# Kernel optimization log

Hardware: AMD Instinct MI355X
Metric: run time of the kernel (lower is better)

Reference implementation:

```python
import jax, jax.numpy as jnp
import numpy as np
from jax import lax

B, L, C = 8, 2048, 512
CR = C // 4      # SE reduction hidden
DH = C // 2      # fusion d_hidden
KS = [3, 7, 15, 20]
EPS = 1e-5


def _ln(x, g, b):
    m = jnp.mean(x, -1, keepdims=True)
    v = jnp.mean((x - m) ** 2, -1, keepdims=True)
    return (x - m) / jnp.sqrt(v + EPS) * g + b


def _bn(x, g, b, m, v):  # x: [B,C,L], eval-mode BatchNorm1d
    return (x - m[:, None]) / jnp.sqrt(v[:, None] + EPS) * g[:, None] + b[:, None]


def _forward(x, pw_w, pw_b, pw_bn_g, pw_bn_b, pw_bn_m, pw_bn_v,
             dw_w0, dw_w1, dw_w2, dw_w3, dw_b, dw_bn_g, dw_bn_b, dw_bn_m, dw_bn_v,
             se_w1, se_b1, se_w2, se_b2, se_ln_g, se_ln_b,
             df_ln_g, df_ln_b, wq, bq, wv, bv, wg, bg,
             op_w, op_b, op_ln_g, op_ln_b, fn_g, fn_b):
    Bs, Ls, Cs = x.shape
    x_in = jnp.transpose(x, (0, 2, 1))                      # [B,C,L]
    # pointwise conv (1x1) + BN + ReLU
    x_pw = jnp.einsum('oc,bcl->bol', pw_w, x_in) + pw_b[:, None]
    x_pw = jax.nn.relu(_bn(x_pw, pw_bn_g, pw_bn_b, pw_bn_m, pw_bn_v))

    enhanced = []
    for i, (w, k) in enumerate(zip([dw_w0, dw_w1, dw_w2, dw_w3], KS)):
        p = (k - 1) // 2
        y = lax.conv_general_dilated(
            x_pw, w[:, None, :], window_strides=(1,), padding=[(p, p)],
            feature_group_count=Cs, dimension_numbers=('NCH', 'OIH', 'NCH'))
        y = y + dw_b[i][:, None]
        y = jax.nn.relu(_bn(y, dw_bn_g[i], dw_bn_b[i], dw_bn_m[i], dw_bn_v[i]))
        if y.shape[2] > Ls:
            y = y[:, :, :Ls]
        elif y.shape[2] < Ls:
            y = jnp.pad(y, ((0, 0), (0, 0), (0, Ls - y.shape[2])))
        feat = jnp.transpose(y, (0, 2, 1))                  # [B,L,C]
        # ChannelAttentionBlock (SE): pool over L -> MLP -> sigmoid gate -> residual LN
        ym = jnp.mean(feat, axis=1)                          # [B,C]
        h = jax.nn.relu(ym @ se_w1[i].T + se_b1[i])          # [B,CR]
        wt = jax.nn.sigmoid(h @ se_w2[i].T + se_b2[i])       # [B,C]
        enhanced.append(_ln(feat + feat * wt[:, None, :], se_ln_g[i], se_ln_b[i]))

    # diff_conv: fixed weight w[:,:,0]=-1, w[:,:,1]=1 => every out channel is
    # sum_c(x[l+1,c]-x[l,c]); pad one zero step at the end
    s = jnp.sum(x[:, 1:] - x[:, :-1], axis=-1, keepdims=True)    # [B,L-1,1]
    diff_feat = jnp.pad(jnp.broadcast_to(s, (Bs, Ls - 1, Cs)), ((0, 0), (0, 1), (0, 0)))

    # DiffGuidedInteractiveFusion
    D = _ln(diff_feat, df_ln_g, df_ln_b)
    Q = D @ wq.T + bq                                       # [B,L,DH]
    scores = []
    for f in enhanced:
        Vi = f @ wv.T + bv                                  # [B,L,DH]
        scores.append(jnp.tanh(Q * Vi) @ wg + bg)           # [B,L]
    scores = jnp.stack(scores, axis=-1)                     # [B,L,S]
    sw = jax.nn.softmax(scores, axis=-1)
    fused = sum(sw[..., i:i + 1] * enhanced[i] for i in range(len(enhanced)))
    out = _ln(fused @ op_w.T + op_b, op_ln_g, op_ln_b)
    return _ln(out + x, fn_g, fn_b)


def setup_inputs() -> dict:
    key = jax.random.key(0)
    ks = jax.random.split(key, 12)
    r = lambda k, s: jax.random.normal(k, s, jnp.float32) * 0.02
    return {
        'x': jax.random.normal(ks[0], (B, L, C), jnp.float32),
        'pw_w': r(ks[1], (C, C)), 'pw_b': jnp.zeros(C),
        'pw_bn_g': jnp.ones(C), 'pw_bn_b': jnp.zeros(C), 'pw_bn_m': jnp.zeros(C), 'pw_bn_v': jnp.ones(C),
        'dw_w0': r(ks[2], (C, 3)), 'dw_w1': r(ks[3], (C, 7)), 'dw_w2': r(ks[4], (C, 15)), 'dw_w3': r(ks[5], (C, 20)),
        'dw_b': jnp.zeros((4, C)),
        'dw_bn_g': jnp.ones((4, C)), 'dw_bn_b': jnp.zeros((4, C)), 'dw_bn_m': jnp.zeros((4, C)), 'dw_bn_v': jnp.ones((4, C)),
        'se_w1': r(ks[6], (4, CR, C)), 'se_b1': jnp.zeros((4, CR)),
        'se_w2': r(ks[7], (4, C, CR)), 'se_b2': jnp.zeros((4, C)),
        'se_ln_g': jnp.ones((4, C)), 'se_ln_b': jnp.zeros((4, C)),
        'df_ln_g': jnp.ones(C), 'df_ln_b': jnp.zeros(C),
        'wq': r(ks[8], (DH, C)), 'bq': jnp.zeros(DH),
        'wv': r(ks[9], (DH, C)), 'bv': jnp.zeros(DH),
        'wg': r(ks[10], (DH,)), 'bg': jnp.zeros(()),
        'op_w': r(ks[11], (C, C)), 'op_b': jnp.zeros(C),
        'op_ln_g': jnp.ones(C), 'op_ln_b': jnp.zeros(C),
        'fn_g': jnp.ones(C), 'fn_b': jnp.zeros(C),
    }


def reference(x, pw_w, pw_b, pw_bn_g, pw_bn_b, pw_bn_m, pw_bn_v,
              dw_w0, dw_w1, dw_w2, dw_w3, dw_b, dw_bn_g, dw_bn_b, dw_bn_m, dw_bn_v,
              se_w1, se_b1, se_w2, se_b2, se_ln_g, se_ln_b,
              df_ln_g, df_ln_b, wq, bq, wv, bv, wg, bg,
              op_w, op_b, op_ln_g, op_ln_b, fn_g, fn_b):
    return _forward(x, pw_w, pw_b, pw_bn_g, pw_bn_b, pw_bn_m, pw_bn_v,
                    dw_w0, dw_w1, dw_w2, dw_w3, dw_b, dw_bn_g, dw_bn_b, dw_bn_m, dw_bn_v,
                    se_w1, se_b1, se_w2, se_b2, se_ln_g, se_ln_b,
                    df_ln_g, df_ln_b, wq, bq, wv, bv, wg, bg,
                    op_w, op_b, op_ln_g, op_ln_b, fn_g, fn_b)
```

## Files before the change

### kernel.cpp

```cpp
#include <hip/hip_runtime.h>
#include <math.h>

static constexpr int Bz = 8;
static constexpr int Lz = 2048;
static constexpr int Cz = 512;
static constexpr int CRz = 128;
static constexpr int DHz = 256;
static constexpr int MT = Bz * Lz;
static constexpr float EPSz = 1e-5f;

typedef unsigned short u16;
typedef __bf16 bf16x8 __attribute__((ext_vector_type(8)));
typedef float f32x4 __attribute__((ext_vector_type(4)));
typedef unsigned short u16x8 __attribute__((ext_vector_type(8)));

__device__ __forceinline__ float bf2f(u16 u) {
  unsigned int v = ((unsigned int)u) << 16;
  return __builtin_bit_cast(float, v);
}
__device__ __forceinline__ u16 f2bf(float f) {
  unsigned int b = __builtin_bit_cast(unsigned int, f);
  b += 0x7FFFu + ((b >> 16) & 1u);
  return (u16)(b >> 16);
}
__device__ __forceinline__ f32x4 mfma16(bf16x8 a, bf16x8 b, f32x4 c) {
  return __builtin_amdgcn_mfma_f32_16x16x32_bf16(a, b, c, 0, 0, 0);
}

__global__ __launch_bounds__(256) void cvt_bf16_kernel(
    const float* __restrict__ src, u16* __restrict__ dst, int n8) {
  int i = blockIdx.x * 256 + threadIdx.x;
  if (i >= n8) return;
  const float4* s = (const float4*)src;
  float4 a = s[i * 2], b = s[i * 2 + 1];
  u16x8 o;
  o[0] = f2bf(a.x); o[1] = f2bf(a.y); o[2] = f2bf(a.z); o[3] = f2bf(a.w);
  o[4] = f2bf(b.x); o[5] = f2bf(b.y); o[6] = f2bf(b.z); o[7] = f2bf(b.w);
  ((u16x8*)dst)[i] = o;
}

__global__ __launch_bounds__(256) void prep_kernel(
    const float* __restrict__ pw_b, const float* __restrict__ pw_g,
    const float* __restrict__ pw_bb, const float* __restrict__ pw_m,
    const float* __restrict__ pw_v,
    const float* __restrict__ dw_b, const float* __restrict__ dw_g,
    const float* __restrict__ dw_bb, const float* __restrict__ dw_m,
    const float* __restrict__ dw_v,
    const float* __restrict__ df_ln_b, const float* __restrict__ wq,
    const float* __restrict__ bq,
    float* __restrict__ pwA, float* __restrict__ pwB,
    float* __restrict__ dwA, float* __restrict__ dwB,
    float* __restrict__ qc) {
  const int blk = blockIdx.x;
  const int t = threadIdx.x;
  if (blk == 0) {
    for (int c = t; c < Cz; c += 256) {
      float inv = rsqrtf(pw_v[c] + EPSz);
      float a = pw_g[c] * inv;
      float bb = pw_bb[c] - pw_m[c] * a;
      pwA[c] = a;
      pwB[c] = pw_b[c] * a + bb;
    }
  } else if (blk <= 4) {
    const int i = blk - 1;
    for (int c = t; c < Cz; c += 256) {
      int idx = i * Cz + c;
      float inv = rsqrtf(dw_v[idx] + EPSz);
      float a = dw_g[idx] * inv;
      float bb = dw_bb[idx] - dw_m[idx] * a;
      dwA[idx] = a;
      dwB[idx] = dw_b[idx] * a + bb;
    }
  } else {
    if (t < DHz) {
      float s = bq[t];
      const float* w = wq + (size_t)t * Cz;
      for (int c = 0; c < Cz; c++) s += df_ln_b[c] * w[c];
      qc[t] = s;
    }
  }
}

__global__ __launch_bounds__(256, 2) void pw_mfma_kernel(
    const u16* __restrict__ Wbf, const float* __restrict__ x,
    const float* __restrict__ alpha, const float* __restrict__ beta,
    u16* __restrict__ xpw) {
  __shared__ __align__(16) char lds[74240];
  u16(*sX)[520] = (u16(*)[520])lds;
  u16(*sW)[40] = (u16(*)[40])(lds + 33280);
  u16* sC = (u16*)(lds + 33280);
  __shared__ float sAl[Cz];
  __shared__ float sBe[Cz];
  const int bat = blockIdx.x >> 6;
  const int l0 = (blockIdx.x & 63) * 32;
  const int t = threadIdx.x;
  const int lane = t & 63, w = t >> 6;
  const int fr = lane & 15, fk = (lane >> 4) * 8;
  const int mh = (w >> 1) * 16;
  const int nh = (w & 1) * 16;
#pragma unroll
  for (int rep = 0; rep < 8; rep++) {
    const int idx = rep * 256 + t;
    const int row = idx >> 6;
    const int col = (idx & 63) * 8;
    const float* src = x + ((size_t)bat * Lz + l0 + row) * Cz + col;
    float4 f0 = *(const float4*)src;
    float4 f1 = *(const float4*)(src + 4);
    u16x8 o;
    o[0] = f2bf(f0.x); o[1] = f2bf(f0.y); o[2] = f2bf(f0.z); o[3] = f2bf(f0.w);
    o[4] = f2bf(f1.x); o[5] = f2bf(f1.y); o[6] = f2bf(f1.z); o[7] = f2bf(f1.w);
    *(u16x8*)&sX[row][col] = o;
  }
  for (int c = t; c < Cz; c += 256) { sAl[c] = alpha[c]; sBe[c] = beta[c]; }
  f32x4 acc[16];
#pragma unroll
  for (int mf = 0; mf < 16; mf++)
#pragma unroll
    for (int r = 0; r < 4; r++) acc[mf][r] = 0.f;
  const int wrow = t >> 2, wch = (t & 3) * 8;
  const u16* wbase = Wbf + (size_t)wrow * Cz + wch;
  u16x8 breg[8];
#pragma unroll
  for (int rep = 0; rep < 8; rep++)
    breg[rep] = *(const u16x8*)(wbase + (size_t)rep * 64 * Cz);
  for (int k0 = 0; k0 < Cz; k0 += 32) {
    __syncthreads();
#pragma unroll
    for (int rep = 0; rep < 8; rep++)
      *(u16x8*)&sW[rep * 64 + wrow][wch] = breg[rep];
    __syncthreads();
    if (k0 + 32 < Cz) {
#pragma unroll
      for (int rep = 0; rep < 8; rep++)
        breg[rep] = *(const u16x8*)(wbase + (size_t)rep * 64 * Cz + k0 + 32);
    }
    bf16x8 bfrag = *(const bf16x8*)&sX[nh + fr][k0 + fk];
#pragma unroll
    for (int mf = 0; mf < 16; mf++) {
      bf16x8 a = *(const bf16x8*)&sW[(mh + mf) * 16 + fr][fk];
      acc[mf] = mfma16(a, bfrag, acc[mf]);
    }
  }
  __syncthreads();
#pragma unroll
  for (int mf = 0; mf < 16; mf++) {
#pragma unroll
    for (int r = 0; r < 4; r++) {
      const int o = (mh + mf) * 16 + ((lane >> 4) << 2) + r;
      const int l = nh + fr;
      float v = fmaxf(acc[mf][r] * sAl[o] + sBe[o], 0.f);
      sC[o * 40 + l] = f2bf(v);
    }
  }
  __syncthreads();
#pragma unroll
  for (int rep = 0; rep < 8; rep++) {
    const int o = rep * 64 + (t >> 2);
    const int l8 = (t & 3) * 8;
    u16x8 v = *(const u16x8*)&sC[o * 40 + l8];
    *(u16x8*)(xpw + ((size_t)(bat * Cz + o)) * Lz + l0 + l8) = v;
  }
}

template <int K>
__device__ __forceinline__ void dw_body(const float* __restrict__ row,
                                        const float* __restrict__ w,
                                        float a, float bb, int valid, int t,
                                        u16* __restrict__ dst, float& psum) {
  constexpr int P = (K - 1) / 2;
  constexpr int W = 8 + K - 1;
  float wreg[K];
#pragma unroll
  for (int j = 0; j < K; j++) wreg[j] = w[j];
  const int base = t * 8 - P;
  float win[W];
  if (base >= 0 && base + W <= Lz) {
#pragma unroll
    for (int j = 0; j < W; j++) win[j] = row[base + j];
  } else {
#pragma unroll
    for (int j = 0; j < W; j++) {
      int xi = base + j;
      win[j] = (xi >= 0 && xi < Lz) ? row[xi] : 0.f;
    }
  }
  float acc[8] = {};
#pragma unroll
  for (int jj = 0; jj < K; jj++)
#pragma unroll
    for (int o = 0; o < 8; o++) acc[o] = fmaf(wreg[jj], win[jj + o], acc[o]);
  u16x8 ov;
#pragma unroll
  for (int o = 0; o < 8; o++) {
    float v = fmaxf(acc[o] * a + bb, 0.f);
    if (t * 8 + o >= valid) v = 0.f;
    ov[o] = f2bf(v);
    psum += v;
  }
  *(u16x8*)(dst + t * 8) = ov;
}

__global__ __launch_bounds__(256) void dw_conv_kernel(
    const u16* __restrict__ xpw,
    const float* __restrict__ w0, const float* __restrict__ w1,
    const float* __restrict__ w2, const float* __restrict__ w3,
    const float* __restrict__ dwA, const float* __restrict__ dwB,
    u16* __restrict__ y, float* __restrict__ ysum) {
  __shared__ float row[Lz];
  __shared__ float wsum[4];
  const int bx = blockIdx.x;
  const int i = bx >> 12;
  const int rem = bx & 4095;
  const int b = rem >> 9;
  const int c = rem & 511;
  const int t = threadIdx.x;
  const u16* src = xpw + ((size_t)(b * Cz + c)) * Lz;
  {
    u16x8 v = ((const u16x8*)src)[t];
#pragma unroll
    for (int j = 0; j < 8; j++) row[t * 8 + j] = bf2f(v[j]);
  }
  __syncthreads();
  const float a = dwA[i * Cz + c], bb = dwB[i * Cz + c];
  u16* dst = y + ((size_t)((i * Bz + b) * Cz + c)) * Lz;
  float psum = 0.f;
  if (i == 0) {
    dw_body<3>(row, w0 + c * 3, a, bb, Lz, t, dst, psum);
  } else if (i == 1) {
    dw_body<7>(row, w1 + c * 7, a, bb, Lz, t, dst, psum);
  } else if (i == 2) {
    dw_body<15>(row, w2 + c * 15, a, bb, Lz, t, dst, psum);
  } else {
    dw_body<20>(row, w3 + c * 20, a, bb, Lz - 1, t, dst, psum);
  }
  for (int off = 32; off > 0; off >>= 1) psum += __shfl_down(psum, off, 64);
  if ((t & 63) == 0) wsum[t >> 6] = psum;
  __syncthreads();
  if (t == 0) ysum[(i * Bz + b) * Cz + c] = wsum[0] + wsum[1] + wsum[2] + wsum[3];
}

__global__ __launch_bounds__(128) void se_kernel(
    const float* __restrict__ ysum,
    const float* __restrict__ se_w1, const float* __restrict__ se_b1,
    const float* __restrict__ se_w2, const float* __restrict__ se_b2,
    float* __restrict__ sc) {
  const int i = blockIdx.x >> 3;
  const int b = blockIdx.x & 7;
  __shared__ float ym[Cz];
  __shared__ float h[CRz];
  const int t = threadIdx.x;
  const float* ys = ysum + (i * Bz + b) * Cz;
  for (int cc = t; cc < Cz; cc += 128) ym[cc] = ys[cc] * (1.f / Lz);
  __syncthreads();
  {
    const float* w1 = se_w1 + (size_t)i * CRz * Cz + (size_t)t * Cz;
    float s = se_b1[i * CRz + t];
    for (int cc = 0; cc < Cz; cc++) s += ym[cc] * w1[cc];
    h[t] = fmaxf(s, 0.f);
  }
  __syncthreads();
  for (int cc = t; cc < Cz; cc += 128) {
    const float* w2 = se_w2 + ((size_t)i * Cz + cc) * CRz;
    float s = se_b2[i * Cz + cc];
    for (int r = 0; r < CRz; r++) s += h[r] * w2[r];
    float wt = 1.f / (1.f + expf(-s));
    sc[(i * Bz + b) * Cz + cc] = 1.f + wt;
  }
}

__global__ __launch_bounds__(256) void ln_transpose_kernel(
    const u16* __restrict__ ybuf, const float* __restrict__ scv,
    const float* __restrict__ se_ln_g, const float* __restrict__ se_ln_b,
    u16* __restrict__ ebuf) {
  __shared__ float tile[32][Cz + 1];
  const size_t NBL = (size_t)Bz * Cz * Lz;
  const int i = blockIdx.y >> 3;
  const int b = blockIdx.y & 7;
  const int l0 = blockIdx.x * 32;
  const int t = threadIdx.x;
  const u16* yb = ybuf + (size_t)i * NBL + (size_t)b * Cz * Lz;
  const float* scb = scv + (i * Bz + b) * Cz;
  const float* g = se_ln_g + i * Cz;
  const float* bb = se_ln_b + i * Cz;
#pragma unroll
  for (int rep = 0; rep < 8; rep++) {
    const int idx = rep * 256 + t;
    const int c = idx >> 2;
    const int l8 = (idx & 3) * 8;
    u16x8 v = *(const u16x8*)(yb + (size_t)c * Lz + l0 + l8);
    const float scale = scb[c];
#pragma unroll
    for (int j = 0; j < 8; j++) tile[l8 + j][c] = bf2f(v[j]) * scale;
  }
  __syncthreads();
  const int wave = t >> 6, lane = t & 63;
  u16* eb = ebuf + (size_t)i * NBL + ((size_t)b * Lz + l0) * Cz;
  for (int r = wave; r < 32; r += 4) {
    float vals[8];
    float s1 = 0.f, s2 = 0.f;
#pragma unroll
    for (int j = 0; j < 8; j++) {
      float v = tile[r][lane + j * 64];
      vals[j] = v; s1 += v; s2 += v * v;
    }
    for (int off = 32; off > 0; off >>= 1) {
      s1 += __shfl_xor(s1, off, 64);
      s2 += __shfl_xor(s2, off, 64);
    }
    const float m = s1 * (1.f / Cz);
    const float var = s2 * (1.f / Cz) - m * m;
    const float inv = rsqrtf(var + EPSz);
#pragma unroll
    for (int j = 0; j < 8; j++) {
      const int cc = lane + j * 64;
      eb[(size_t)r * Cz + cc] = f2bf((vals[j] - m) * inv * g[cc] + bb[cc]);
    }
  }
}

__global__ __launch_bounds__(256) void score_mfma_kernel(
    const u16* __restrict__ e0, const u16* __restrict__ e1,
    const u16* __restrict__ e2, const u16* __restrict__ e3,
    const u16* __restrict__ wvbf, const float* __restrict__ bv,
    const float* __restrict__ qc, const float* __restrict__ wg,
    const float* __restrict__ bg, float* __restrict__ scores) {
  __shared__ u16 sA[64][40];
  __shared__ u16 sB[256][40];
  __shared__ float sP[4][64];
  const int i = blockIdx.y;
  const u16* E = (i == 0) ? e0 : (i == 1) ? e1 : (i == 2) ? e2 : e3;
  const int r0 = blockIdx.x * 64;
  const int t = threadIdx.x;
  const int lane = t & 63, w = t >> 6;
  const int srow = t >> 2, skoff = (t & 3) * 8;
  const int fr = lane & 15, fk = (lane >> 4) * 8;
  const u16* ap = E + (size_t)(r0 + srow) * Cz + skoff;
  const u16* bp = wvbf + (size_t)srow * Cz + skoff;
  f32x4 acc[4][4];
#pragma unroll
  for (int m = 0; m < 4; m++)
#pragma unroll
    for (int j = 0; j < 4; j++)
#pragma unroll
      for (int r = 0; r < 4; r++) acc[m][j][r] = 0.f;
  for (int k0 = 0; k0 < Cz; k0 += 32) {
    u16x8 av = *(const u16x8*)(ap + k0);
    u16x8 bq0 = *(const u16x8*)(bp + k0);
    u16x8 bq1 = *(const u16x8*)(bp + (size_t)64 * Cz + k0);
    u16x8 bq2 = *(const u16x8*)(bp + (size_t)128 * Cz + k0);
    u16x8 bq3 = *(const u16x8*)(bp + (size_t)192 * Cz + k0);
    __syncthreads();
    *(u16x8*)&sA[srow][skoff] = av;
    *(u16x8*)&sB[srow][skoff] = bq0;
    *(u16x8*)&sB[srow + 64][skoff] = bq1;
    *(u16x8*)&sB[srow + 128][skoff] = bq2;
    *(u16x8*)&sB[srow + 192][skoff] = bq3;
    __syncthreads();
    bf16x8 am[4], bj[4];
#pragma unroll
    for (int m = 0; m < 4; m++) am[m] = *(const bf16x8*)&sA[m * 16 + fr][fk];
#pragma unroll
    for (int j = 0; j < 4; j++)
      bj[j] = *(const bf16x8*)&sB[(w * 4 + j) * 16 + fr][fk];
#pragma unroll
    for (int m = 0; m < 4; m++)
#pragma unroll
      for (int j = 0; j < 4; j++)
        acc[m][j] = mfma16(am[m], bj[j], acc[m][j]);
  }
  float part[4][4];
#pragma unroll
  for (int m = 0; m < 4; m++)
#pragma unroll
    for (int r = 0; r < 4; r++) part[m][r] = 0.f;
#pragma unroll
  for (int j = 0; j < 4; j++) {
    const int dh = (w * 4 + j) * 16 + fr;
    const float bvn = bv[dh], qcn = qc[dh], wgn = wg[dh];
#pragma unroll
    for (int m = 0; m < 4; m++)
#pragma unroll
      for (int r = 0; r < 4; r++)
        part[m][r] += tanhf(qcn * (acc[m][j][r] + bvn)) * wgn;
  }
#pragma unroll
  for (int off = 1; off < 16; off <<= 1) {
#pragma unroll
    for (int m = 0; m < 4; m++)
#pragma unroll
      for (int r = 0; r < 4; r++)
        part[m][r] += __shfl_xor(part[m][r], off, 64);
  }
  if (fr == 0) {
#pragma unroll
    for (int m = 0; m < 4; m++)
#pragma unroll
      for (int r = 0; r < 4; r++)
        sP[w][m * 16 + ((lane >> 4) << 2) + r] = part[m][r];
  }
  __syncthreads();
  if (t < 64) {
    float s = sP[0][t] + sP[1][t] + sP[2][t] + sP[3][t] + bg[0];
    scores[(size_t)i * MT + r0 + t] = s;
  }
}

__global__ __launch_bounds__(256, 2) void op_mfma_kernel(
    const u16* __restrict__ e0, const u16* __restrict__ e1,
    const u16* __restrict__ e2, const u16* __restrict__ e3,
    const float* __restrict__ scores, const u16* __restrict__ opwbf,
    const float* __restrict__ opb, u16* __restrict__ oproj) {
  __shared__ u16 sA[32][520];
  __shared__ u16 sB[512][40];
  __shared__ float sw4[4][32];
  const int m0 = blockIdx.x * 32;
  const int t = threadIdx.x;
  const int lane = t & 63, w = t >> 6;
  const int fr = lane & 15, fk = (lane >> 4) * 8;
  const int mh = (w >> 1) * 16;
  const int nh = (w & 1) * 16;
  if (t < 32) {
    const int r = m0 + t;
    float s0 = scores[r], s1 = scores[MT + r], s2 = scores[2 * MT + r],
          s3 = scores[3 * MT + r];
    float mx = fmaxf(fmaxf(s0, s1), fmaxf(s2, s3));
    float x0 = expf(s0 - mx), x1 = expf(s1 - mx), x2 = expf(s2 - mx),
          x3 = expf(s3 - mx);
    float inv = 1.f / (x0 + x1 + x2 + x3);
    sw4[0][t] = x0 * inv; sw4[1][t] = x1 * inv;
    sw4[2][t] = x2 * inv; sw4[3][t] = x3 * inv;
  }
  __syncthreads();
#pragma unroll
  for (int rep = 0; rep < 8; rep++) {
    const int idx = rep * 256 + t;
    const int row = idx >> 6;
    const int col = (idx & 63) * 8;
    const size_t off = (size_t)(m0 + row) * Cz + col;
    u16x8 v0 = *(const u16x8*)(e0 + off);
    u16x8 v1 = *(const u16x8*)(e1 + off);
    u16x8 v2 = *(const u16x8*)(e2 + off);
    u16x8 v3 = *(const u16x8*)(e3 + off);
    const float x0 = sw4[0][row], x1 = sw4[1][row], x2 = sw4[2][row],
                x3 = sw4[3][row];
    u16x8 o;
#pragma unroll
    for (int j = 0; j < 8; j++)
      o[j] = f2bf(x0 * bf2f(v0[j]) + x1 * bf2f(v1[j]) + x2 * bf2f(v2[j]) +
                  x3 * bf2f(v3[j]));
    *(u16x8*)&sA[row][col] = o;
  }
  f32x4 acc[16];
#pragma unroll
  for (int nf = 0; nf < 16; nf++)
#pragma unroll
    for (int r = 0; r < 4; r++) acc[nf][r] = 0.f;
  const int wrow = t >> 2, wch = (t & 3) * 8;
  const u16* wbase = opwbf + (size_t)wrow * Cz + wch;
  u16x8 breg[8];
#pragma unroll
  for (int rep = 0; rep < 8; rep++)
    breg[rep] = *(const u16x8*)(wbase + (size_t)rep * 64 * Cz);
  for (int k0 = 0; k0 < Cz; k0 += 32) {
    __syncthreads();
#pragma unroll
    for (int rep = 0; rep < 8; rep++)
      *(u16x8*)&sB[rep * 64 + wrow][wch] = breg[rep];
    __syncthreads();
    if (k0 + 32 < Cz) {
#pragma unroll
      for (int rep = 0; rep < 8; rep++)
        breg[rep] = *(const u16x8*)(wbase + (size_t)rep * 64 * Cz + k0 + 32);
    }
    bf16x8 a = *(const bf16x8*)&sA[mh + fr][k0 + fk];
#pragma unroll
    for (int nf = 0; nf < 16; nf++) {
      bf16x8 b = *(const bf16x8*)&sB[(nh + nf) * 16 + fr][fk];
      acc[nf] = mfma16(a, b, acc[nf]);
    }
  }
  __syncthreads();
  u16* sC = (u16*)&sA[0][0];
#pragma unroll
  for (int nf = 0; nf < 16; nf++) {
    const int n = (nh + nf) * 16 + fr;
    const float ob = opb[n];
#pragma unroll
    for (int r = 0; r < 4; r++) {
      const int row = mh + ((lane >> 4) << 2) + r;
      sC[row * 520 + n] = f2bf(acc[nf][r] + ob);
    }
  }
  __syncthreads();
#pragma unroll
  for (int rep = 0; rep < 8; rep++) {
    const int idx = rep * 256 + t;
    const int row = idx >> 6;
    const int col = (idx & 63) * 8;
    u16x8 v = *(const u16x8*)&sC[row * 520 + col];
    *(u16x8*)(oproj + (size_t)(m0 + row) * Cz + col) = v;
  }
}

__global__ __launch_bounds__(256) void final_ln_kernel(
    const u16* __restrict__ oproj, const float* __restrict__ g1,
    const float* __restrict__ b1, const float* __restrict__ x,
    const float* __restrict__ g2, const float* __restrict__ b2,
    float* __restrict__ out) {
  const int t = threadIdx.x;
  const int row = blockIdx.x * 4 + (t >> 6);
  const int lane = t & 63;
  u16x8 av = ((const u16x8*)(oproj + (size_t)row * Cz))[lane];
  float v[8];
  float s1 = 0.f, s2 = 0.f;
#pragma unroll
  for (int j = 0; j < 8; j++) {
    v[j] = bf2f(av[j]);
    s1 += v[j]; s2 += v[j] * v[j];
  }
  for (int off = 1; off < 64; off <<= 1) {
    s1 += __shfl_xor(s1, off, 64);
    s2 += __shfl_xor(s2, off, 64);
  }
  const float m1 = s1 * (1.f / Cz);
  const float iv1 = rsqrtf(s2 * (1.f / Cz) - m1 * m1 + EPSz);
  float4 g1a = ((const float4*)g1)[lane * 2], g1b = ((const float4*)g1)[lane * 2 + 1];
  float4 b1a = ((const float4*)b1)[lane * 2], b1b = ((const float4*)b1)[lane * 2 + 1];
  const float* xr = x + (size_t)row * Cz;
  float4 xa = ((const float4*)xr)[lane * 2], xb = ((const float4*)xr)[lane * 2 + 1];
  float gv[8] = {g1a.x, g1a.y, g1a.z, g1a.w, g1b.x, g1b.y, g1b.z, g1b.w};
  float bvv[8] = {b1a.x, b1a.y, b1a.z, b1a.w, b1b.x, b1b.y, b1b.z, b1b.w};
  float xv[8] = {xa.x, xa.y, xa.z, xa.w, xb.x, xb.y, xb.z, xb.w};
  float tv[8];
  s1 = 0.f; s2 = 0.f;
#pragma unroll
  for (int j = 0; j < 8; j++) {
    tv[j] = (v[j] - m1) * iv1 * gv[j] + bvv[j] + xv[j];
    s1 += tv[j]; s2 += tv[j] * tv[j];
  }
  for (int off = 1; off < 64; off <<= 1) {
    s1 += __shfl_xor(s1, off, 64);
    s2 += __shfl_xor(s2, off, 64);
  }
  const float m2 = s1 * (1.f / Cz);
  const float iv2 = rsqrtf(s2 * (1.f / Cz) - m2 * m2 + EPSz);
  float4 g2a = ((const float4*)g2)[lane * 2], g2b = ((const float4*)g2)[lane * 2 + 1];
  float4 b2a = ((const float4*)b2)[lane * 2], b2b = ((const float4*)b2)[lane * 2 + 1];
  float g2v[8] = {g2a.x, g2a.y, g2a.z, g2a.w, g2b.x, g2b.y, g2b.z, g2b.w};
  float b2v[8] = {b2a.x, b2a.y, b2a.z, b2a.w, b2b.x, b2b.y, b2b.z, b2b.w};
  float4 oa, ob;
  oa.x = (tv[0] - m2) * iv2 * g2v[0] + b2v[0];
  oa.y = (tv[1] - m2) * iv2 * g2v[1] + b2v[1];
  oa.z = (tv[2] - m2) * iv2 * g2v[2] + b2v[2];
  oa.w = (tv[3] - m2) * iv2 * g2v[3] + b2v[3];
  ob.x = (tv[4] - m2) * iv2 * g2v[4] + b2v[4];
  ob.y = (tv[5] - m2) * iv2 * g2v[5] + b2v[5];
  ob.z = (tv[6] - m2) * iv2 * g2v[6] + b2v[6];
  ob.w = (tv[7] - m2) * iv2 * g2v[7] + b2v[7];
  float* orow = out + (size_t)row * Cz;
  ((float4*)orow)[lane * 2] = oa;
  ((float4*)orow)[lane * 2 + 1] = ob;
}

extern "C" void kernel_launch(void* const* d_in, const int* in_sizes, int n_in,
                              void* d_out, int out_size, void* d_ws,
                              size_t ws_size, hipStream_t stream) {
  const float* x = (const float*)d_in[0];
  const float* pw_w = (const float*)d_in[1];
  const float* pw_b = (const float*)d_in[2];
  const float* pw_bn_g = (const float*)d_in[3];
  const float* pw_bn_b = (const float*)d_in[4];
  const float* pw_bn_m = (const float*)d_in[5];
  const float* pw_bn_v = (const float*)d_in[6];
  const float* dw_w0 = (const float*)d_in[7];
  const float* dw_w1 = (const float*)d_in[8];
  const float* dw_w2 = (const float*)d_in[9];
  const float* dw_w3 = (const float*)d_in[10];
  const float* dw_b = (const float*)d_in[11];
  const float* dw_bn_g = (const float*)d_in[12];
  const float* dw_bn_b = (const float*)d_in[13];
  const float* dw_bn_m = (const float*)d_in[14];
  const float* dw_bn_v = (const float*)d_in[15];
  const float* se_w1 = (const float*)d_in[16];
  const float* se_b1 = (const float*)d_in[17];
  const float* se_w2 = (const float*)d_in[18];
  const float* se_b2 = (const float*)d_in[19];
  const float* se_ln_g = (const float*)d_in[20];
  const float* se_ln_b = (const float*)d_in[21];
  const float* df_ln_b = (const float*)d_in[23];
  const float* wq = (const float*)d_in[24];
  const float* bq = (const float*)d_in[25];
  const float* wv = (const float*)d_in[26];
  const float* bv = (const float*)d_in[27];
  const float* wg = (const float*)d_in[28];
  const float* bg = (const float*)d_in[29];
  const float* op_w = (const float*)d_in[30];
  const float* op_b = (const float*)d_in[31];
  const float* op_ln_g = (const float*)d_in[32];
  const float* op_ln_b = (const float*)d_in[33];
  const float* fn_g = (const float*)d_in[34];
  const float* fn_b = (const float*)d_in[35];
  float* out = (float*)d_out;

  const size_t NBL = (size_t)Bz * Cz * Lz;
  char* p = (char*)d_ws;
  u16* oproj = (u16*)p; p += NBL * 2;
  u16* xpw = (u16*)p; p += NBL * 2;
  u16* ybuf = (u16*)p; p += 4 * NBL * 2;
  u16* ebuf = (u16*)p; p += 4 * NBL * 2;
  u16* pwwbf = (u16*)p; p += (size_t)Cz * Cz * 2;
  u16* wvbf = (u16*)p; p += (size_t)DHz * Cz * 2;
  u16* opwbf = (u16*)p; p += (size_t)Cz * Cz * 2;
  float* fbuf = (float*)p;
  float* ysum = fbuf;
  float* scv = fbuf + 16384;
  float* scores = fbuf + 32768;
  float* pwA = fbuf + 98304;
  float* pwB = pwA + 512;
  float* dwA = pwB + 512;
  float* dwB = dwA + 2048;
  float* qc = dwB + 2048;

  cvt_bf16_kernel<<<Cz * Cz / 8 / 256, 256, 0, stream>>>(pw_w, pwwbf,
                                                         Cz * Cz / 8);
  cvt_bf16_kernel<<<DHz * Cz / 8 / 256, 256, 0, stream>>>(wv, wvbf,
                                                          DHz * Cz / 8);
  cvt_bf16_kernel<<<Cz * Cz / 8 / 256, 256, 0, stream>>>(op_w, opwbf,
                                                         Cz * Cz / 8);

  prep_kernel<<<6, 256, 0, stream>>>(pw_b, pw_bn_g, pw_bn_b, pw_bn_m, pw_bn_v,
                                     dw_b, dw_bn_g, dw_bn_b, dw_bn_m, dw_bn_v,
                                     df_ln_b, wq, bq, pwA, pwB, dwA, dwB, qc);

  pw_mfma_kernel<<<Bz * (Lz / 32), 256, 0, stream>>>(pwwbf, x, pwA, pwB, xpw);

  dw_conv_kernel<<<4 * Bz * Cz, 256, 0, stream>>>(xpw, dw_w0, dw_w1, dw_w2,
                                                  dw_w3, dwA, dwB, ybuf, ysum);

  se_kernel<<<32, 128, 0, stream>>>(ysum, se_w1, se_b1, se_w2, se_b2, scv);

  ln_transpose_kernel<<<dim3(Lz / 32, 4 * Bz), 256, 0, stream>>>(
      ybuf, scv, se_ln_g, se_ln_b, ebuf);

  score_mfma_kernel<<<dim3(MT / 64, 4), 256, 0, stream>>>(
      ebuf, ebuf + NBL, ebuf + 2 * NBL, ebuf + 3 * NBL, wvbf, bv, qc, wg, bg,
      scores);

  op_mfma_kernel<<<MT / 32, 256, 0, stream>>>(
      ebuf, ebuf + NBL, ebuf + 2 * NBL, ebuf + 3 * NBL, scores, opwbf, op_b,
      oproj);

  final_ln_kernel<<<MT / 4, 256, 0, stream>>>(oproj, op_ln_g, op_ln_b, x, fn_g,
                                              fn_b, out);
}
```

Before: 252.0 us.

## Compute all four depthwise conv branches per block from one shared row load

The depthwise conv kernel now runs one block per (batch, channel) and computes all four kernel-size branches from a single bf16 row staged in shared memory. Previously each branch launched its own block and reloaded the same row. The weights for all branches are staged in shared memory, and the row is padded by one word every 32 floats to cut LDS bank conflicts on the strided window reads. This removes three quarters of the xpw reads and block launches, but each block does more serial work and holds more registers, and the grid shrinks fourfold, which lowers parallelism.

Result: faster. 236.4 us (-6.2%).

```diff
diff --git a/kernel.cpp b/kernel.cpp
--- a/kernel.cpp
+++ b/kernel.cpp
@@ -163,25 +163,28 @@
 }
 
 template <int K>
-__device__ __forceinline__ void dw_body(const float* __restrict__ row,
-                                        const float* __restrict__ w,
-                                        float a, float bb, int valid, int t,
-                                        u16* __restrict__ dst, float& psum) {
+__device__ __forceinline__ float dw_branch(const float* __restrict__ row,
+                                           const float* __restrict__ wts,
+                                           float a, float bb, int valid, int t,
+                                           u16* __restrict__ dst) {
   constexpr int P = (K - 1) / 2;
   constexpr int W = 8 + K - 1;
   float wreg[K];
 #pragma unroll
-  for (int j = 0; j < K; j++) wreg[j] = w[j];
+  for (int j = 0; j < K; j++) wreg[j] = wts[j];
   const int base = t * 8 - P;
   float win[W];
   if (base >= 0 && base + W <= Lz) {
 #pragma unroll
-    for (int j = 0; j < W; j++) win[j] = row[base + j];
+    for (int j = 0; j < W; j++) {
+      const int idx = base + j;
+      win[j] = row[idx + (idx >> 5)];
+    }
   } else {
 #pragma unroll
     for (int j = 0; j < W; j++) {
-      int xi = base + j;
-      win[j] = (xi >= 0 && xi < Lz) ? row[xi] : 0.f;
+      const int idx = base + j;
+      win[j] = (idx >= 0 && idx < Lz) ? row[idx + (idx >> 5)] : 0.f;
     }
   }
   float acc[8] = {};
@@ -190,6 +193,7 @@
 #pragma unroll
     for (int o = 0; o < 8; o++) acc[o] = fmaf(wreg[jj], win[jj + o], acc[o]);
   u16x8 ov;
+  float psum = 0.f;
 #pragma unroll
   for (int o = 0; o < 8; o++) {
     float v = fmaxf(acc[o] * a + bb, 0.f);
@@ -198,6 +202,7 @@
     psum += v;
   }
   *(u16x8*)(dst + t * 8) = ov;
+  return psum;
 }
 
 __global__ __launch_bounds__(256) void dw_conv_kernel(
@@ -206,37 +211,52 @@
     const float* __restrict__ w2, const float* __restrict__ w3,
     const float* __restrict__ dwA, const float* __restrict__ dwB,
     u16* __restrict__ y, float* __restrict__ ysum) {
-  __shared__ float row[Lz];
-  __shared__ float wsum[4];
-  const int bx = blockIdx.x;
-  const int i = bx >> 12;
-  const int rem = bx & 4095;
-  const int b = rem >> 9;
-  const int c = rem & 511;
-  const int t = threadIdx.x;
-  const u16* src = xpw + ((size_t)(b * Cz + c)) * Lz;
+  __shared__ float row[Lz + Lz / 32];
+  __shared__ float wts[48];
+  __shared__ float wsum[4][4];
+  const int b = blockIdx.x >> 9;
+  const int c = blockIdx.x & 511;
+  const int t = threadIdx.x;
+  const size_t NBL = (size_t)Bz * Cz * Lz;
   {
-    u16x8 v = ((const u16x8*)src)[t];
-#pragma unroll
-    for (int j = 0; j < 8; j++) row[t * 8 + j] = bf2f(v[j]);
-  }
-  __syncthreads();
-  const float a = dwA[i * Cz + c], bb = dwB[i * Cz + c];
-  u16* dst = y + ((size_t)((i * Bz + b) * Cz + c)) * Lz;
-  float psum = 0.f;
-  if (i == 0) {
-    dw_body<3>(row, w0 + c * 3, a, bb, Lz, t, dst, psum);
-  } else if (i == 1) {
-    dw_body<7>(row, w1 + c * 7, a, bb, Lz, t, dst, psum);
-  } else if (i == 2) {
-    dw_body<15>(row, w2 + c * 15, a, bb, Lz, t, dst, psum);
-  } else {
-    dw_body<20>(row, w3 + c * 20, a, bb, Lz - 1, t, dst, psum);
-  }
-  for (int off = 32; off > 0; off >>= 1) psum += __shfl_down(psum, off, 64);
-  if ((t & 63) == 0) wsum[t >> 6] = psum;
-  __syncthreads();
-  if (t == 0) ysum[(i * Bz + b) * Cz + c] = wsum[0] + wsum[1] + wsum[2] + wsum[3];
+    u16x8 v = ((const u16x8*)(xpw + ((size_t)(b * Cz + c)) * Lz))[t];
+#pragma unroll
+    for (int j = 0; j < 8; j++) {
+      const int idx = t * 8 + j;
+      row[idx + (idx >> 5)] = bf2f(v[j]);
+    }
+  }
+  if (t < 45) {
+    float wv;
+    if (t < 3) wv = w0[c * 3 + t];
+    else if (t < 10) wv = w1[c * 7 + (t - 3)];
+    else if (t < 25) wv = w2[c * 15 + (t - 10)];
+    else wv = w3[c * 20 + (t - 25)];
+    wts[t] = wv;
+  }
+  __syncthreads();
+  u16* dstb = y + ((size_t)b * Cz + c) * Lz;
+  float ps[4];
+  ps[0] = dw_branch<3>(row, wts + 0, dwA[c], dwB[c], Lz, t, dstb);
+  ps[1] = dw_branch<7>(row, wts + 3, dwA[Cz + c], dwB[Cz + c], Lz, t,
+                       dstb + NBL);
+  ps[2] = dw_branch<15>(row, wts + 10, dwA[2 * Cz + c], dwB[2 * Cz + c], Lz, t,
+                        dstb + 2 * NBL);
+  ps[3] = dw_branch<20>(row, wts + 25, dwA[3 * Cz + c], dwB[3 * Cz + c],
+                        Lz - 1, t, dstb + 3 * NBL);
+#pragma unroll
+  for (int off = 32; off > 0; off >>= 1) {
+#pragma unroll
+    for (int i = 0; i < 4; i++) ps[i] += __shfl_down(ps[i], off, 64);
+  }
+  if ((t & 63) == 0) {
+#pragma unroll
+    for (int i = 0; i < 4; i++) wsum[t >> 6][i] = ps[i];
+  }
+  __syncthreads();
+  if (t < 4)
+    ysum[(t * Bz + b) * Cz + c] =
+        wsum[0][t] + wsum[1][t] + wsum[2][t] + wsum[3][t];
 }
 
 __global__ __launch_bounds__(128) void se_kernel(
@@ -634,8 +654,8 @@
 
   pw_mfma_kernel<<<Bz * (Lz / 32), 256, 0, stream>>>(pwwbf, x, pwA, pwB, xpw);
 
-  dw_conv_kernel<<<4 * Bz * Cz, 256, 0, stream>>>(xpw, dw_w0, dw_w1, dw_w2,
-                                                  dw_w3, dwA, dwB, ybuf, ysum);
+  dw_conv_kernel<<<Bz * Cz, 256, 0, stream>>>(xpw, dw_w0, dw_w1, dw_w2, dw_w3,
+                                              dwA, dwB, ybuf, ysum);
 
   se_kernel<<<32, 128, 0, stream>>>(ysum, se_w1, se_b1, se_w2, se_b2, scv);
 
```
